# Performance work log

Measured on AMD Instinct MI355X. Metric: run time of the kernel, lower is better.

## Reference

```python
import jax, jax.numpy as jnp
import numpy as np

D_MODEL = 1024
N_HEAD = 16
HEAD_SIZE = D_MODEL // N_HEAD
SEQ = 2048
BATCH = 4
LN_EPS = 1e-5


def layer_norm(x, gamma, beta):
    mu = jnp.mean(x, axis=-1, keepdims=True)
    var = jnp.var(x, axis=-1, keepdims=True)
    return (x - mu) * jax.lax.rsqrt(var + LN_EPS) * gamma + beta


def setup_inputs() -> dict:
    key = jax.random.key(0)
    ks = jax.random.split(key, 12)
    s = 0.02
    return {
        "x": jax.random.normal(ks[0], (BATCH, SEQ, D_MODEL), jnp.float32),
        "Wq": jax.random.normal(ks[1], (N_HEAD, D_MODEL, HEAD_SIZE), jnp.float32) * s,
        "Wk": jax.random.normal(ks[2], (N_HEAD, D_MODEL, HEAD_SIZE), jnp.float32) * s,
        "Wv": jax.random.normal(ks[3], (N_HEAD, D_MODEL, HEAD_SIZE), jnp.float32) * s,
        "Wo": jax.random.normal(ks[4], (D_MODEL, D_MODEL), jnp.float32) * s,
        "bo": jnp.zeros((D_MODEL,), jnp.float32),
        "W1": jax.random.normal(ks[5], (D_MODEL, 4 * D_MODEL), jnp.float32) * s,
        "b1": jnp.zeros((4 * D_MODEL,), jnp.float32),
        "W2": jax.random.normal(ks[6], (4 * D_MODEL, D_MODEL), jnp.float32) * s,
        "b2": jnp.zeros((D_MODEL,), jnp.float32),
        "g1": jnp.ones((D_MODEL,), jnp.float32),
        "be1": jnp.zeros((D_MODEL,), jnp.float32),
        "g2": jnp.ones((D_MODEL,), jnp.float32),
        "be2": jnp.zeros((D_MODEL,), jnp.float32),
    }


def reference(x, Wq, Wk, Wv, Wo, bo, W1, b1, W2, b2, g1, be1, g2, be2):
    B, T, C = x.shape
    # --- self-attention branch (dropout = eval identity) ---
    h = layer_norm(x, g1, be1)
    q = jnp.einsum('btc,hcs->bhts', h, Wq)
    k = jnp.einsum('btc,hcs->bhts', h, Wk)
    v = jnp.einsum('btc,hcs->bhts', h, Wv)
    wei = jnp.einsum('bhts,bhus->bhtu', q, k) * (HEAD_SIZE ** -0.5)
    # non-standard diagonal mask: scores on the diagonal are set to 0 (not -inf)
    diag = jnp.eye(T, dtype=bool)
    wei = jnp.where(diag, jnp.zeros((), wei.dtype), wei)
    wei = jax.nn.softmax(wei, axis=-1)
    att = jnp.einsum('bhtu,bhus->bhts', wei, v)          # [B,H,T,hs]
    att = att.transpose(0, 2, 1, 3).reshape(B, T, C)      # concat heads
    sa = att @ Wo + bo
    x = x + sa
    # --- feed-forward branch ---
    h2 = layer_norm(x, g2, be2)
    ff = jax.nn.gelu(h2 @ W1 + b1, approximate=False) @ W2 + b2
    return x + ff
```

## Files before the change

### kernel.cpp

```cpp
#include <hip/hip_runtime.h>
#include <hip/hip_bf16.h>
#include <math.h>

#define D_MODEL 1024
#define N_HEAD 16
#define HEAD 64
#define SEQ 2048
#define BATCH 4
#define ROWS (BATCH*SEQ)
#define FFD 4096

typedef __bf16 bf16;
typedef __attribute__((ext_vector_type(8))) __bf16 bf16x8;
typedef __attribute__((ext_vector_type(4))) __bf16 bf16x4;
typedef __attribute__((ext_vector_type(4))) float f32x4;
typedef __attribute__((ext_vector_type(16))) float f32x16;
typedef __attribute__((ext_vector_type(4))) short short4v;

static_assert(sizeof(bf16x8) == 16, "bf16x8 must be 16B");

__device__ __forceinline__ void async_copy16(const void* g, void* l) {
  __builtin_amdgcn_global_load_lds((const __attribute__((address_space(1))) void*)g,
                                   (__attribute__((address_space(3))) void*)l, 16, 0, 0);
}

__device__ __forceinline__ f32x4 mfma16(bf16x8 a, bf16x8 b, f32x4 c) {
  return __builtin_amdgcn_mfma_f32_16x16x32_bf16(a, b, c, 0, 0, 0);
}

__device__ __forceinline__ f32x16 mfma32(bf16x8 a, bf16x8 b, f32x16 c) {
  return __builtin_amdgcn_mfma_f32_32x32x16_bf16(a, b, c, 0, 0, 0);
}

__device__ __forceinline__ f32x4 mfma16k16(bf16x4 a, bf16x4 b, f32x4 c) {
#if __has_builtin(__builtin_amdgcn_mfma_f32_16x16x16_bf16)
  return __builtin_amdgcn_mfma_f32_16x16x16_bf16(a, b, c, 0, 0, 0);
#else
  return __builtin_amdgcn_mfma_f32_16x16x16bf16_1k(__builtin_bit_cast(short4v, a),
                                                   __builtin_bit_cast(short4v, b), c, 0, 0, 0);
#endif
}

__device__ __forceinline__ float fast_exp2(float x) {
#if __has_builtin(__builtin_amdgcn_exp2f)
  return __builtin_amdgcn_exp2f(x);
#else
  float r; asm("v_exp_f32 %0, %1" : "=v"(r) : "v"(x)); return r;
#endif
}

__device__ __forceinline__ float fast_gelu(float x) {
  const float y = 0.7978845608f * (x + 0.044715f * x * x * x);
  const float e = fast_exp2(y * 2.88539008178f);
  return 0.5f * x * (1.f + (1.f - 2.f / (e + 1.f)));
}

__global__ __launch_bounds__(256) void transpose_cast_kernel(const float* __restrict__ in,
                                                             bf16* __restrict__ out,
                                                             int R, int C) {
  __shared__ float ts[32][33];
  const int r0 = blockIdx.y * 32, c0 = blockIdx.x * 32;
  const int t = threadIdx.x, lr = t >> 3, lc = (t & 7) * 4;
  const float4 v = *(const float4*)(in + (size_t)(r0 + lr) * C + c0 + lc);
  ts[lr][lc + 0] = v.x; ts[lr][lc + 1] = v.y; ts[lr][lc + 2] = v.z; ts[lr][lc + 3] = v.w;
  __syncthreads();
  bf16x4 o;
  o[0] = (bf16)ts[lc + 0][lr]; o[1] = (bf16)ts[lc + 1][lr];
  o[2] = (bf16)ts[lc + 2][lr]; o[3] = (bf16)ts[lc + 3][lr];
  *(bf16x4*)(out + (size_t)(c0 + lr) * R + r0 + lc) = o;
}

__global__ __launch_bounds__(256) void qkv_transpose_kernel(const float* __restrict__ Wq,
                                                            const float* __restrict__ Wk,
                                                            const float* __restrict__ Wv,
                                                            bf16* __restrict__ out) {
  __shared__ float ts[32][33];
  const int mat = blockIdx.z / N_HEAD, h = blockIdx.z % N_HEAD;
  const float* W = (mat == 0 ? Wq : mat == 1 ? Wk : Wv) + (size_t)h * D_MODEL * HEAD;
  bf16* o = out + (size_t)mat * D_MODEL * D_MODEL + (size_t)(h * HEAD) * D_MODEL;
  const int c0 = blockIdx.x * 32, s0 = blockIdx.y * 32;
  const int t = threadIdx.x, lr = t >> 3, lc = (t & 7) * 4;
  const float4 v = *(const float4*)(W + (size_t)(c0 + lr) * HEAD + s0 + lc);
  ts[lr][lc + 0] = v.x; ts[lr][lc + 1] = v.y; ts[lr][lc + 2] = v.z; ts[lr][lc + 3] = v.w;
  __syncthreads();
  bf16x4 ov;
  ov[0] = (bf16)ts[lc + 0][lr]; ov[1] = (bf16)ts[lc + 1][lr];
  ov[2] = (bf16)ts[lc + 2][lr]; ov[3] = (bf16)ts[lc + 3][lr];
  *(bf16x4*)(o + (size_t)(s0 + lr) * D_MODEL + c0 + lc) = ov;
}

__global__ __launch_bounds__(256) void ln_kernel(const float* __restrict__ x,
                                                 const float* __restrict__ g,
                                                 const float* __restrict__ b,
                                                 bf16* __restrict__ h) {
  const int row = blockIdx.x, t = threadIdx.x;
  const float4 v = *(const float4*)(x + (size_t)row * D_MODEL + t * 4);
  float s = v.x + v.y + v.z + v.w;
  float ss = v.x * v.x + v.y * v.y + v.z * v.z + v.w * v.w;
#pragma unroll
  for (int m = 1; m < 64; m <<= 1) { s += __shfl_xor(s, m); ss += __shfl_xor(ss, m); }
  __shared__ float red[8];
  const int wave = t >> 6, lane = t & 63;
  if (lane == 0) { red[wave] = s; red[4 + wave] = ss; }
  __syncthreads();
  s = red[0] + red[1] + red[2] + red[3];
  ss = red[4] + red[5] + red[6] + red[7];
  const float mu = s * (1.f / D_MODEL);
  const float rstd = rsqrtf(ss * (1.f / D_MODEL) - mu * mu + 1e-5f);
  const float4 gv = *(const float4*)(g + t * 4);
  const float4 bv = *(const float4*)(b + t * 4);
  bf16x4 o;
  o[0] = (bf16)((v.x - mu) * rstd * gv.x + bv.x);
  o[1] = (bf16)((v.y - mu) * rstd * gv.y + bv.y);
  o[2] = (bf16)((v.z - mu) * rstd * gv.z + bv.z);
  o[3] = (bf16)((v.w - mu) * rstd * gv.w + bv.w);
  *(bf16x4*)(h + (size_t)row * D_MODEL + t * 4) = o;
}

template <int EPI>
__global__ __launch_bounds__(256) void gemm_kernel(const bf16* __restrict__ A,
                                                   const bf16* __restrict__ Bt, int K,
                                                   void* __restrict__ outp,
                                                   const float* __restrict__ bias,
                                                   const float* __restrict__ resid,
                                                   bf16* __restrict__ q_out,
                                                   bf16* __restrict__ k_out,
                                                   bf16* __restrict__ vt_out, int N) {
  __shared__ bf16 As[128 * 64];
  __shared__ bf16 Bs[128 * 64];
  const int t = threadIdx.x;
  const int bm = blockIdx.y, bn = blockIdx.x;
  const int srow = t >> 3;
  const int schunk = (t & 7) ^ (srow & 7);
  const bf16* Ag = A + (size_t)(bm * 128 + srow) * K + schunk * 8;
  const bf16* Bg = Bt + (size_t)(bn * 128 + srow) * K + schunk * 8;
  bf16* Asd = As + t * 8;
  bf16* Bsd = Bs + t * 8;

  const int wave = t >> 6, lane = t & 63, l31 = lane & 31, lk = lane >> 5;
  const int wm = (wave >> 1) * 64, wn = (wave & 1) * 64;

  f32x16 acc[2][2];
#pragma unroll
  for (int i = 0; i < 2; i++)
#pragma unroll
    for (int j = 0; j < 2; j++)
#pragma unroll
      for (int e = 0; e < 16; e++) acc[i][j][e] = 0.f;

  for (int kt = 0; kt < K; kt += 64) {
    __syncthreads();
#pragma unroll
    for (int i = 0; i < 4; i++) {
      async_copy16(Ag + kt + (size_t)(32 * i) * K, Asd + 2048 * i);
      async_copy16(Bg + kt + (size_t)(32 * i) * K, Bsd + 2048 * i);
    }
    __syncthreads();
#pragma unroll
    for (int s = 0; s < 4; s++) {
      const int pos = ((s << 1) | lk) ^ (l31 & 7);
      bf16x8 af[2], bfr[2];
#pragma unroll
      for (int i = 0; i < 2; i++) af[i] = *(const bf16x8*)(As + (wm + i * 32 + l31) * 64 + pos * 8);
#pragma unroll
      for (int j = 0; j < 2; j++) bfr[j] = *(const bf16x8*)(Bs + (wn + j * 32 + l31) * 64 + pos * 8);
#pragma unroll
      for (int i = 0; i < 2; i++)
#pragma unroll
        for (int j = 0; j < 2; j++) acc[i][j] = mfma32(af[i], bfr[j], acc[i][j]);
    }
  }

#pragma unroll
  for (int i = 0; i < 2; i++) {
#pragma unroll
    for (int j = 0; j < 2; j++) {
      const int n = bn * 128 + wn + j * 32 + l31;
#pragma unroll
      for (int e = 0; e < 16; e++) {
        const int m = bm * 128 + wm + i * 32 + (e & 3) + 8 * (e >> 2) + 4 * lk;
        float val = acc[i][j][e];
        if constexpr (EPI == 0) {
          const int b = m >> 11, tt = m & 2047;
          if (n < D_MODEL) {
            const int hh = n >> 6, sgl = n & 63;
            q_out[(size_t)((b * N_HEAD + hh) * SEQ + tt) * HEAD + sgl] = (bf16)val;
          } else if (n < 2 * D_MODEL) {
            const int n2 = n - D_MODEL, hh = n2 >> 6, sgl = n2 & 63;
            k_out[(size_t)((b * N_HEAD + hh) * SEQ + tt) * HEAD + sgl] = (bf16)val;
          } else {
            const int n2 = n - 2 * D_MODEL, hh = n2 >> 6, sgl = n2 & 63;
            vt_out[(size_t)((b * N_HEAD + hh) * HEAD + sgl) * SEQ + tt] = (bf16)val;
          }
        } else if constexpr (EPI == 1) {
          ((float*)outp)[(size_t)m * N + n] = val + bias[n] + resid[(size_t)m * N + n];
        } else if constexpr (EPI == 2) {
          ((bf16*)outp)[(size_t)m * N + n] = (bf16)fast_gelu(val + bias[n]);
        } else {
          ((float*)outp)[(size_t)m * N + n] = val + bias[n] + resid[(size_t)m * N + n];
        }
      }
    }
  }
}

__global__ __launch_bounds__(256, 2) void attn_kernel(const bf16* __restrict__ q,
                                                      const bf16* __restrict__ k,
                                                      const bf16* __restrict__ vt,
                                                      bf16* __restrict__ att) {
  __shared__ bf16 Ks[64 * 64];
  __shared__ bf16 Vs[64 * 64];
  const int t = threadIdx.x, wave = t >> 6, lane = t & 63;
  const int l15 = lane & 15, l4 = lane >> 4;
  const int bh = blockIdx.x & 63, qblk = blockIdx.x >> 6;
  const bf16* qb = q + (size_t)bh * SEQ * HEAD;
  const bf16* kb = k + (size_t)bh * SEQ * HEAD;
  const bf16* vb = vt + (size_t)bh * HEAD * SEQ;
  const int qrow = qblk * 256 + wave * 64;

  const int tr = t >> 3, tc = t & 7, sw = tc ^ (tr & 7);
  const bf16* ksrc0 = kb + (size_t)tr * HEAD + sw * 8;
  const bf16* ksrc1 = kb + (size_t)(tr + 32) * HEAD + sw * 8;
  const bf16* vsrc0 = vb + (size_t)tr * SEQ + sw * 8;
  const bf16* vsrc1 = vb + (size_t)(tr + 32) * SEQ + sw * 8;
  bf16* kd0 = Ks + t * 8; bf16* kd1 = Ks + t * 8 + 2048;
  bf16* vd0 = Vs + t * 8; bf16* vd1 = Vs + t * 8 + 2048;

  const float qscale = 0.125f * 1.44269504088896340736f;
  bf16x8 qf[4][2];
#pragma unroll
  for (int qs = 0; qs < 4; qs++)
#pragma unroll
    for (int h = 0; h < 2; h++) {
      const bf16x8 raw = *(const bf16x8*)(qb + (size_t)(qrow + qs * 16 + l15) * HEAD + h * 32 + l4 * 8);
      bf16x8 sc;
#pragma unroll
      for (int e = 0; e < 8; e++) sc[e] = (bf16)((float)raw[e] * qscale);
      qf[qs][h] = sc;
    }

  f32x4 o[4][4];
  float lsum[4] = {0.f, 0.f, 0.f, 0.f};
#pragma unroll
  for (int qs = 0; qs < 4; qs++)
#pragma unroll
    for (int dm = 0; dm < 4; dm++) { f32x4 z = {0.f, 0.f, 0.f, 0.f}; o[qs][dm] = z; }

  const int rsw = l15 & 7;

  for (int u0 = 0; u0 < SEQ; u0 += 64) {
    __syncthreads();
    async_copy16(ksrc0 + (size_t)u0 * HEAD, kd0);
    async_copy16(ksrc1 + (size_t)u0 * HEAD, kd1);
    async_copy16(vsrc0 + u0, vd0);
    async_copy16(vsrc1 + u0, vd1);
    __syncthreads();

    bf16x8 kf[4][2];
#pragma unroll
    for (int n = 0; n < 4; n++)
#pragma unroll
      for (int h = 0; h < 2; h++)
        kf[n][h] = *(const bf16x8*)(Ks + (n * 16 + l15) * 64 + (((h << 2) | l4) ^ rsw) * 8);
    bf16x4 vf[4][4];
#pragma unroll
    for (int dm = 0; dm < 4; dm++)
#pragma unroll
      for (int n = 0; n < 4; n++)
        vf[dm][n] = *(const bf16x4*)(Vs + (dm * 16 + l15) * 64 + ((((n << 1) | (l4 >> 1)) ^ rsw) * 8) + (l4 & 1) * 4);

#pragma unroll
    for (int qs = 0; qs < 4; qs++) {
      f32x4 s[4];
#pragma unroll
      for (int n = 0; n < 4; n++) {
        f32x4 c = {0.f, 0.f, 0.f, 0.f};
        c = mfma16(kf[n][0], qf[qs][0], c);
        c = mfma16(kf[n][1], qf[qs][1], c);
        s[n] = c;
      }
      if (u0 == qrow) {
#pragma unroll
        for (int r = 0; r < 4; r++)
          s[qs][r] = (l15 == l4 * 4 + r) ? 0.f : s[qs][r];
      }
      bf16x4 pf[4];
      float ls = 0.f;
#pragma unroll
      for (int n = 0; n < 4; n++) {
        f32x4 pv;
#pragma unroll
        for (int r = 0; r < 4; r++) { pv[r] = fast_exp2(s[n][r]); ls += pv[r]; }
        bf16x4 pb;
#pragma unroll
        for (int r = 0; r < 4; r++) pb[r] = (bf16)pv[r];
        pf[n] = pb;
      }
      lsum[qs] += ls;
#pragma unroll
      for (int dm = 0; dm < 4; dm++) {
        f32x4 acc = o[qs][dm];
#pragma unroll
        for (int n = 0; n < 4; n++) acc = mfma16k16(vf[dm][n], pf[n], acc);
        o[qs][dm] = acc;
      }
    }
  }

#pragma unroll
  for (int qs = 0; qs < 4; qs++) {
    float l = lsum[qs];
    l += __shfl_xor(l, 16);
    l += __shfl_xor(l, 32);
    lsum[qs] = l;
  }
  const int b = bh >> 4, hh = bh & 15;
#pragma unroll
  for (int qs = 0; qs < 4; qs++) {
    const float linv = 1.0f / lsum[qs];
#pragma unroll
    for (int dm = 0; dm < 4; dm++) {
      bf16x4 ov;
#pragma unroll
      for (int r = 0; r < 4; r++) ov[r] = (bf16)(o[qs][dm][r] * linv);
      *(bf16x4*)(att + (size_t)(b * SEQ + qrow + qs * 16 + l15) * D_MODEL + hh * HEAD + dm * 16 + l4 * 4) = ov;
    }
  }
}

extern "C" void kernel_launch(void* const* d_in, const int* in_sizes, int n_in,
                              void* d_out, int out_size, void* d_ws, size_t ws_size,
                              hipStream_t stream) {
  const float* x   = (const float*)d_in[0];
  const float* Wq  = (const float*)d_in[1];
  const float* Wk  = (const float*)d_in[2];
  const float* Wv  = (const float*)d_in[3];
  const float* Wo  = (const float*)d_in[4];
  const float* bo  = (const float*)d_in[5];
  const float* W1  = (const float*)d_in[6];
  const float* b1  = (const float*)d_in[7];
  const float* W2  = (const float*)d_in[8];
  const float* b2  = (const float*)d_in[9];
  const float* g1  = (const float*)d_in[10];
  const float* be1 = (const float*)d_in[11];
  const float* g2  = (const float*)d_in[12];
  const float* be2 = (const float*)d_in[13];
  float* out = (float*)d_out;

  bf16* Wqkv_t = (bf16*)d_ws;
  bf16* Wo_t   = Wqkv_t + (size_t)3 * D_MODEL * D_MODEL;
  bf16* W1_t   = Wo_t + (size_t)D_MODEL * D_MODEL;
  bf16* W2_t   = W1_t + (size_t)FFD * D_MODEL;
  bf16* hbuf   = W2_t + (size_t)D_MODEL * FFD;
  float* x1    = (float*)(hbuf + (size_t)ROWS * D_MODEL);
  bf16* big    = (bf16*)(x1 + (size_t)ROWS * D_MODEL);
  bf16* qbuf   = big;
  bf16* kbuf   = qbuf + (size_t)ROWS * D_MODEL;
  bf16* vtbuf  = kbuf + (size_t)ROWS * D_MODEL;
  bf16* ffbuf  = big;
  bf16* attb   = big + (size_t)ROWS * FFD;

  qkv_transpose_kernel<<<dim3(D_MODEL / 32, HEAD / 32, 3 * N_HEAD), 256, 0, stream>>>(Wq, Wk, Wv, Wqkv_t);
  transpose_cast_kernel<<<dim3(D_MODEL / 32, D_MODEL / 32), 256, 0, stream>>>(Wo, Wo_t, D_MODEL, D_MODEL);
  transpose_cast_kernel<<<dim3(FFD / 32, D_MODEL / 32), 256, 0, stream>>>(W1, W1_t, D_MODEL, FFD);
  transpose_cast_kernel<<<dim3(D_MODEL / 32, FFD / 32), 256, 0, stream>>>(W2, W2_t, FFD, D_MODEL);
  ln_kernel<<<ROWS, 256, 0, stream>>>(x, g1, be1, hbuf);
  gemm_kernel<0><<<dim3(3 * D_MODEL / 128, ROWS / 128), 256, 0, stream>>>(
      hbuf, Wqkv_t, D_MODEL, nullptr, nullptr, nullptr, qbuf, kbuf, vtbuf, 3 * D_MODEL);
  attn_kernel<<<64 * (SEQ / 256), 256, 0, stream>>>(qbuf, kbuf, vtbuf, attb);
  gemm_kernel<1><<<dim3(D_MODEL / 128, ROWS / 128), 256, 0, stream>>>(
      attb, Wo_t, D_MODEL, x1, bo, x, nullptr, nullptr, nullptr, D_MODEL);
  ln_kernel<<<ROWS, 256, 0, stream>>>(x1, g2, be2, hbuf);
  gemm_kernel<2><<<dim3(FFD / 128, ROWS / 128), 256, 0, stream>>>(
      hbuf, W1_t, D_MODEL, ffbuf, b1, nullptr, nullptr, nullptr, nullptr, FFD);
  gemm_kernel<3><<<dim3(D_MODEL / 128, ROWS / 128), 256, 0, stream>>>(
      ffbuf, W2_t, FFD, out, b2, x1, nullptr, nullptr, nullptr, D_MODEL);
}
```

Before: 536.0 us.

## Rewrite GEMMs with 256-wide tiles, double-buffered async staging and 16x16 MFMA

Replaces the 128x128 single-buffered GEMM with a templated body using 256- or 128-row by 256-column tiles, 512 threads, and double-buffered LDS filled by async global-to-LDS copies that are interleaved with the MFMA phases. It adds a blockIdx swizzle for L2 locality, uses s_setprio around the MFMA bursts, and switches from 32x32 to 16x16x32 MFMAs. The aim is to hide global load latency and improve data reuse across all four GEMMs. In exchange it uses more LDS and registers and relies on hand-placed waitcnt and barrier ordering, which is fragile.

```diff
diff --git a/kernel.cpp b/kernel.cpp
--- a/kernel.cpp
+++ b/kernel.cpp
@@ -14,7 +14,6 @@
 typedef __attribute__((ext_vector_type(8))) __bf16 bf16x8;
 typedef __attribute__((ext_vector_type(4))) __bf16 bf16x4;
 typedef __attribute__((ext_vector_type(4))) float f32x4;
-typedef __attribute__((ext_vector_type(16))) float f32x16;
 typedef __attribute__((ext_vector_type(4))) short short4v;
 
 static_assert(sizeof(bf16x8) == 16, "bf16x8 must be 16B");
@@ -26,10 +25,6 @@
 
 __device__ __forceinline__ f32x4 mfma16(bf16x8 a, bf16x8 b, f32x4 c) {
   return __builtin_amdgcn_mfma_f32_16x16x32_bf16(a, b, c, 0, 0, 0);
-}
-
-__device__ __forceinline__ f32x16 mfma32(bf16x8 a, bf16x8 b, f32x16 c) {
-  return __builtin_amdgcn_mfma_f32_32x32x16_bf16(a, b, c, 0, 0, 0);
 }
 
 __device__ __forceinline__ f32x4 mfma16k16(bf16x4 a, bf16x4 b, f32x4 c) {
@@ -117,69 +112,150 @@
   *(bf16x4*)(h + (size_t)row * D_MODEL + t * 4) = o;
 }
 
-template <int EPI>
-__global__ __launch_bounds__(256) void gemm_kernel(const bf16* __restrict__ A,
-                                                   const bf16* __restrict__ Bt, int K,
-                                                   void* __restrict__ outp,
-                                                   const float* __restrict__ bias,
-                                                   const float* __restrict__ resid,
-                                                   bf16* __restrict__ q_out,
-                                                   bf16* __restrict__ k_out,
-                                                   bf16* __restrict__ vt_out, int N) {
-  __shared__ bf16 As[128 * 64];
-  __shared__ bf16 Bs[128 * 64];
-  const int t = threadIdx.x;
-  const int bm = blockIdx.y, bn = blockIdx.x;
-  const int srow = t >> 3;
-  const int schunk = (t & 7) ^ (srow & 7);
-  const bf16* Ag = A + (size_t)(bm * 128 + srow) * K + schunk * 8;
-  const bf16* Bg = Bt + (size_t)(bn * 128 + srow) * K + schunk * 8;
-  bf16* Asd = As + t * 8;
-  bf16* Bsd = Bs + t * 8;
-
-  const int wave = t >> 6, lane = t & 63, l31 = lane & 31, lk = lane >> 5;
-  const int wm = (wave >> 1) * 64, wn = (wave & 1) * 64;
-
-  f32x16 acc[2][2];
-#pragma unroll
-  for (int i = 0; i < 2; i++)
-#pragma unroll
-    for (int j = 0; j < 2; j++)
-#pragma unroll
-      for (int e = 0; e < 16; e++) acc[i][j][e] = 0.f;
-
-  for (int kt = 0; kt < K; kt += 64) {
-    __syncthreads();
-#pragma unroll
-    for (int i = 0; i < 4; i++) {
-      async_copy16(Ag + kt + (size_t)(32 * i) * K, Asd + 2048 * i);
-      async_copy16(Bg + kt + (size_t)(32 * i) * K, Bsd + 2048 * i);
-    }
-    __syncthreads();
-#pragma unroll
-    for (int s = 0; s < 4; s++) {
-      const int pos = ((s << 1) | lk) ^ (l31 & 7);
-      bf16x8 af[2], bfr[2];
-#pragma unroll
-      for (int i = 0; i < 2; i++) af[i] = *(const bf16x8*)(As + (wm + i * 32 + l31) * 64 + pos * 8);
-#pragma unroll
-      for (int j = 0; j < 2; j++) bfr[j] = *(const bf16x8*)(Bs + (wn + j * 32 + l31) * 64 + pos * 8);
-#pragma unroll
-      for (int i = 0; i < 2; i++)
-#pragma unroll
-        for (int j = 0; j < 2; j++) acc[i][j] = mfma32(af[i], bfr[j], acc[i][j]);
-    }
+#define STAGE_A(kt2, h)                                                          \
+  do {                                                                           \
+    const int off_ = (kt2) * 64 + (h) * 32;                                      \
+    bf16* d_ = aDst0 + (((kt2) & 1) * 2 + (h)) * AHALF;                          \
+    async_copy16(aSrc0 + off_, d_);                                              \
+    if (ASTEPS == 2) async_copy16(aSrc1 + off_, d_ + 4096);                      \
+  } while (0)
+
+#define STAGE_B(kt2, h)                                                          \
+  do {                                                                           \
+    const int off_ = (kt2) * 64 + (h) * 32;                                      \
+    bf16* d_ = bDst0 + (((kt2) & 1) * 2 + (h)) * 8192;                           \
+    async_copy16(bSrc0 + off_, d_);                                              \
+    async_copy16(bSrc1 + off_, d_ + 4096);                                       \
+  } while (0)
+
+template <int EPI, int BM>
+__device__ __forceinline__ void gemm_body(const bf16* A, const bf16* Bt, int K,
+                                          void* outp, const float* bias,
+                                          const float* resid, bf16* q_out,
+                                          bf16* k_out, bf16* vt_out, int N) {
+  constexpr int ASTEPS = BM / 128;
+  constexpr int MPW = BM / 2;
+  constexpr int MREP = MPW / 16;
+  constexpr int AHALF = BM * 32;
+  __shared__ bf16 As[2 * 2 * BM * 32];
+  __shared__ bf16 Bs[2 * 2 * 256 * 32];
+  const int t = threadIdx.x, wave = t >> 6, lane = t & 63;
+  const int l15 = lane & 15, l4 = lane >> 4;
+  const int lin = ((int)blockIdx.x & 7) * ((int)gridDim.x >> 3) + ((int)blockIdx.x >> 3);
+  const int nbn = N >> 8;
+  const int bn = lin % nbn, bm = lin / nbn;
+  const int nk = K >> 6;
+
+  const int sc = (lane & 3) ^ ((lane >> 3) & 3);
+  const int r0 = wave * 16 + (lane >> 2);
+  const bf16* aSrc0 = A + (size_t)(bm * BM + r0) * K + sc * 8;
+  const bf16* aSrc1 = (ASTEPS == 2) ? (A + (size_t)(bm * BM + 128 + r0) * K + sc * 8) : aSrc0;
+  const bf16* bSrc0 = Bt + (size_t)(bn * 256 + r0) * K + sc * 8;
+  const bf16* bSrc1 = Bt + (size_t)(bn * 256 + 128 + r0) * K + sc * 8;
+  bf16* aDst0 = As + wave * 512;
+  bf16* bDst0 = Bs + wave * 512;
+
+  const int wm = wave >> 2, wn = wave & 3;
+  const int rw = wm * MPW, cw = wn * 64;
+  const int pc = (l4 ^ ((l15 >> 1) & 3)) * 8;
+
+  f32x4 acc[MREP][4];
+#pragma unroll
+  for (int mi = 0; mi < MREP; mi++)
+#pragma unroll
+    for (int ni = 0; ni < 4; ni++) { f32x4 z = {0.f, 0.f, 0.f, 0.f}; acc[mi][ni] = z; }
+
+  STAGE_A(0, 0); STAGE_B(0, 0); STAGE_A(0, 1); STAGE_B(0, 1);
+  STAGE_A(1, 0); STAGE_B(1, 0); STAGE_A(1, 1);
+  if constexpr (ASTEPS == 2) asm volatile("s_waitcnt vmcnt(6)" ::: "memory");
+  else                       asm volatile("s_waitcnt vmcnt(4)" ::: "memory");
+  __builtin_amdgcn_s_barrier();
+  __builtin_amdgcn_sched_barrier(0);
+
+  for (int kt = 0; kt < nk; kt++) {
+    const bf16* Ab = As + (kt & 1) * (2 * AHALF);
+    const bf16* Bb = Bs + (kt & 1) * (2 * 8192);
+    bf16x8 aF[MREP], b0, b1;
+
+#pragma unroll
+    for (int mi = 0; mi < MREP; mi++)
+      aF[mi] = *(const bf16x8*)(Ab + (rw + mi * 16 + l15) * 32 + pc);
+    b0 = *(const bf16x8*)(Bb + (cw + l15) * 32 + pc);
+    b1 = *(const bf16x8*)(Bb + (cw + 16 + l15) * 32 + pc);
+    if (kt + 1 < nk) STAGE_B(kt + 1, 1);
+    __builtin_amdgcn_s_barrier();
+    asm volatile("s_waitcnt lgkmcnt(0)" ::: "memory");
+    __builtin_amdgcn_s_setprio(1);
+#pragma unroll
+    for (int mi = 0; mi < MREP; mi++) {
+      acc[mi][0] = mfma16(aF[mi], b0, acc[mi][0]);
+      acc[mi][1] = mfma16(aF[mi], b1, acc[mi][1]);
+    }
+    __builtin_amdgcn_s_setprio(0);
+    __builtin_amdgcn_s_barrier();
+
+    b0 = *(const bf16x8*)(Bb + (cw + 32 + l15) * 32 + pc);
+    b1 = *(const bf16x8*)(Bb + (cw + 48 + l15) * 32 + pc);
+    if (kt + 2 < nk) STAGE_A(kt + 2, 0);
+    __builtin_amdgcn_s_barrier();
+    asm volatile("s_waitcnt lgkmcnt(0)" ::: "memory");
+    __builtin_amdgcn_s_setprio(1);
+#pragma unroll
+    for (int mi = 0; mi < MREP; mi++) {
+      acc[mi][2] = mfma16(aF[mi], b0, acc[mi][2]);
+      acc[mi][3] = mfma16(aF[mi], b1, acc[mi][3]);
+    }
+    __builtin_amdgcn_s_setprio(0);
+    __builtin_amdgcn_s_barrier();
+
+#pragma unroll
+    for (int mi = 0; mi < MREP; mi++)
+      aF[mi] = *(const bf16x8*)(Ab + AHALF + (rw + mi * 16 + l15) * 32 + pc);
+    b0 = *(const bf16x8*)(Bb + 8192 + (cw + l15) * 32 + pc);
+    b1 = *(const bf16x8*)(Bb + 8192 + (cw + 16 + l15) * 32 + pc);
+    if (kt + 2 < nk) STAGE_B(kt + 2, 0);
+    __builtin_amdgcn_s_barrier();
+    asm volatile("s_waitcnt lgkmcnt(0)" ::: "memory");
+    __builtin_amdgcn_s_setprio(1);
+#pragma unroll
+    for (int mi = 0; mi < MREP; mi++) {
+      acc[mi][0] = mfma16(aF[mi], b0, acc[mi][0]);
+      acc[mi][1] = mfma16(aF[mi], b1, acc[mi][1]);
+    }
+    __builtin_amdgcn_s_setprio(0);
+    __builtin_amdgcn_s_barrier();
+
+    b0 = *(const bf16x8*)(Bb + 8192 + (cw + 32 + l15) * 32 + pc);
+    b1 = *(const bf16x8*)(Bb + 8192 + (cw + 48 + l15) * 32 + pc);
+    if (kt + 2 < nk) {
+      STAGE_A(kt + 2, 1);
+      if constexpr (ASTEPS == 2) asm volatile("s_waitcnt vmcnt(6)" ::: "memory");
+      else                       asm volatile("s_waitcnt vmcnt(4)" ::: "memory");
+    } else {
+      asm volatile("s_waitcnt vmcnt(0)" ::: "memory");
+    }
+    __builtin_amdgcn_s_barrier();
+    asm volatile("s_waitcnt lgkmcnt(0)" ::: "memory");
+    __builtin_amdgcn_s_setprio(1);
+#pragma unroll
+    for (int mi = 0; mi < MREP; mi++) {
+      acc[mi][2] = mfma16(aF[mi], b0, acc[mi][2]);
+      acc[mi][3] = mfma16(aF[mi], b1, acc[mi][3]);
+    }
+    __builtin_amdgcn_s_setprio(0);
+    __builtin_amdgcn_s_barrier();
+    __builtin_amdgcn_sched_barrier(0);
   }
 
 #pragma unroll
-  for (int i = 0; i < 2; i++) {
-#pragma unroll
-    for (int j = 0; j < 2; j++) {
-      const int n = bn * 128 + wn + j * 32 + l31;
-#pragma unroll
-      for (int e = 0; e < 16; e++) {
-        const int m = bm * 128 + wm + i * 32 + (e & 3) + 8 * (e >> 2) + 4 * lk;
-        float val = acc[i][j][e];
+  for (int mi = 0; mi < MREP; mi++) {
+#pragma unroll
+    for (int ni = 0; ni < 4; ni++) {
+      const int n = bn * 256 + cw + ni * 16 + l15;
+#pragma unroll
+      for (int e = 0; e < 4; e++) {
+        const int m = bm * BM + rw + mi * 16 + l4 * 4 + e;
+        float val = acc[mi][ni][e];
         if constexpr (EPI == 0) {
           const int b = m >> 11, tt = m & 2047;
           if (n < D_MODEL) {
@@ -204,6 +280,40 @@
   }
 }
 
+#undef STAGE_A
+#undef STAGE_B
+
+__global__ __launch_bounds__(512, 2) void gemm_qkv_kernel(const bf16* __restrict__ A,
+                                                          const bf16* __restrict__ Bt,
+                                                          bf16* __restrict__ q_out,
+                                                          bf16* __restrict__ k_out,
+                                                          bf16* __restrict__ vt_out) {
+  gemm_body<0, 256>(A, Bt, D_MODEL, nullptr, nullptr, nullptr, q_out, k_out, vt_out, 3 * D_MODEL);
+}
+
+__global__ __launch_bounds__(512, 2) void gemm_proj_kernel(const bf16* __restrict__ A,
+                                                           const bf16* __restrict__ Bt,
+                                                           float* __restrict__ outp,
+                                                           const float* __restrict__ bias,
+                                                           const float* __restrict__ resid) {
+  gemm_body<1, 128>(A, Bt, D_MODEL, outp, bias, resid, nullptr, nullptr, nullptr, D_MODEL);
+}
+
+__global__ __launch_bounds__(512, 2) void gemm_ff1_kernel(const bf16* __restrict__ A,
+                                                          const bf16* __restrict__ Bt,
+                                                          bf16* __restrict__ outp,
+                                                          const float* __restrict__ bias) {
+  gemm_body<2, 256>(A, Bt, D_MODEL, outp, bias, nullptr, nullptr, nullptr, nullptr, FFD);
+}
+
+__global__ __launch_bounds__(512, 2) void gemm_ff2_kernel(const bf16* __restrict__ A,
+                                                          const bf16* __restrict__ Bt,
+                                                          float* __restrict__ outp,
+                                                          const float* __restrict__ bias,
+                                                          const float* __restrict__ resid) {
+  gemm_body<3, 128>(A, Bt, FFD, outp, bias, resid, nullptr, nullptr, nullptr, D_MODEL);
+}
+
 __global__ __launch_bounds__(256, 2) void attn_kernel(const bf16* __restrict__ q,
                                                       const bf16* __restrict__ k,
                                                       const bf16* __restrict__ vt,
@@ -365,14 +475,14 @@
   transpose_cast_kernel<<<dim3(FFD / 32, D_MODEL / 32), 256, 0, stream>>>(W1, W1_t, D_MODEL, FFD);
   transpose_cast_kernel<<<dim3(D_MODEL / 32, FFD / 32), 256, 0, stream>>>(W2, W2_t, FFD, D_MODEL);
   ln_kernel<<<ROWS, 256, 0, stream>>>(x, g1, be1, hbuf);
-  gemm_kernel<0><<<dim3(3 * D_MODEL / 128, ROWS / 128), 256, 0, stream>>>(
-      hbuf, Wqkv_t, D_MODEL, nullptr, nullptr, nullptr, qbuf, kbuf, vtbuf, 3 * D_MODEL);
+  gemm_qkv_kernel<<<dim3((3 * D_MODEL / 256) * (ROWS / 256)), 512, 0, stream>>>(
+      hbuf, Wqkv_t, qbuf, kbuf, vtbuf);
   attn_kernel<<<64 * (SEQ / 256), 256, 0, stream>>>(qbuf, kbuf, vtbuf, attb);
-  gemm_kernel<1><<<dim3(D_MODEL / 128, ROWS / 128), 256, 0, stream>>>(
-      attb, Wo_t, D_MODEL, x1, bo, x, nullptr, nullptr, nullptr, D_MODEL);
+  gemm_proj_kernel<<<dim3((D_MODEL / 256) * (ROWS / 128)), 512, 0, stream>>>(
+      attb, Wo_t, x1, bo, x);
   ln_kernel<<<ROWS, 256, 0, stream>>>(x1, g2, be2, hbuf);
-  gemm_kernel<2><<<dim3(FFD / 128, ROWS / 128), 256, 0, stream>>>(
-      hbuf, W1_t, D_MODEL, ffbuf, b1, nullptr, nullptr, nullptr, nullptr, FFD);
-  gemm_kernel<3><<<dim3(D_MODEL / 128, ROWS / 128), 256, 0, stream>>>(
-      ffbuf, W2_t, FFD, out, b2, x1, nullptr, nullptr, nullptr, D_MODEL);
-}
+  gemm_ff1_kernel<<<dim3((FFD / 256) * (ROWS / 256)), 512, 0, stream>>>(
+      hbuf, W1_t, ffbuf, b1);
+  gemm_ff2_kernel<<<dim3((D_MODEL / 256) * (ROWS / 128)), 512, 0, stream>>>(
+      ffbuf, W2_t, out, b2, x1);
+}
```

Result: slower. 592.1 us (+10.5%).
